# Kernel tuning notes

Measured on AMD Instinct MI355X. Metric: run time of the kernel, lower is better.

## Reference

```python
import math
import jax, jax.numpy as jnp
import numpy as np

L, H, K, NH, V, DFF = 6, 512, 512, 8, 64, 1024
B, T, S = 8, 512, 512
PAD = 0


def _ln(x, g, b, eps=1e-5):
    m = jnp.mean(x, -1, keepdims=True)
    v = jnp.mean((x - m) ** 2, -1, keepdims=True)
    return (x - m) * jax.lax.rsqrt(v + eps) * g + b


def _mha(Q, Kin, Vin, mask, wq, bq, wk, bk, wv, bv, wo, bo, g, b):
    # weights stored [in, out]
    B_, Tq, Hd = Q.shape
    dk = wq.shape[1] // NH
    dv = wv.shape[1] // NH
    q = (Q @ wq + bq).reshape(B_, Tq, NH, dk).transpose(0, 2, 1, 3)
    k = (Kin @ wk + bk).reshape(B_, -1, NH, dk).transpose(0, 2, 1, 3)
    v = (Vin @ wv + bv).reshape(B_, -1, NH, dv).transpose(0, 2, 1, 3)
    scores = jnp.einsum('bhqd,bhkd->bhqk', q, k) / jnp.sqrt(jnp.float32(dk))
    scores = jnp.where(mask[:, None, :, :], jnp.float32(-1e9), scores)
    attn = jax.nn.softmax(scores, axis=-1)
    ctx = jnp.einsum('bhqk,bhkd->bhqd', attn, v).transpose(0, 2, 1, 3).reshape(B_, Tq, Hd)
    return _ln(ctx @ wo + bo + Q, g, b)


def _pe(t, d):
    pos = jnp.arange(t, dtype=jnp.float32)[:, None]
    div = jnp.exp(jnp.arange(0, d, 2, dtype=jnp.float32) * (-math.log(10000.0) / d))
    pe = jnp.zeros((t, d), jnp.float32)
    pe = pe.at[:, 0::2].set(jnp.sin(pos * div)).at[:, 1::2].set(jnp.cos(pos * div))
    return pe


def setup_inputs() -> dict:
    key = jax.random.key(0)
    ks = iter(jax.random.split(key, 40))
    nrm = lambda shape, s=0.02: jax.random.normal(next(ks), shape, jnp.float32) * s
    inp = {
        'smiles_index': jax.random.randint(next(ks), (B, T), 0, V, dtype=jnp.int32),
        'enc_outputs': jax.random.normal(next(ks), (B, S, H), jnp.float32),
        'enc_pad_mask': jnp.zeros((B, 1, S), bool),
        'tgt_len': T,
        'mol_emb': nrm((V, H), 1.0).at[PAD].set(0.0),  # padding_idx=0 row zeroed
        # self-attn stacks [L, ...]
        'sa_wq': nrm((L, H, K)), 'sa_bq': jnp.zeros((L, K)),
        'sa_wk': nrm((L, H, K)), 'sa_bk': jnp.zeros((L, K)),
        'sa_wv': nrm((L, H, H)), 'sa_bv': jnp.zeros((L, H)),
        'sa_wo': nrm((L, H, H)), 'sa_bo': jnp.zeros((L, H)),
        'ln1_g': jnp.ones((L, H)), 'ln1_b': jnp.zeros((L, H)),
        # cross-attn stacks
        'ea_wq': nrm((L, H, K)), 'ea_bq': jnp.zeros((L, K)),
        'ea_wk': nrm((L, H, K)), 'ea_bk': jnp.zeros((L, K)),
        'ea_wv': nrm((L, H, H)), 'ea_bv': jnp.zeros((L, H)),
        'ea_wo': nrm((L, H, H)), 'ea_bo': jnp.zeros((L, H)),
        'ln2_g': jnp.ones((L, H)), 'ln2_b': jnp.zeros((L, H)),
        # conv1x1 FFN == per-position linear
        'c1_w': nrm((L, H, DFF)), 'c1_b': jnp.zeros((L, DFF)),
        'c2_w': nrm((L, DFF, H)), 'c2_b': jnp.zeros((L, H)),
        'ln3_g': jnp.ones((L, H)), 'ln3_b': jnp.zeros((L, H)),
    }
    return inp


def reference(smiles_index, enc_outputs, enc_pad_mask, tgt_len, mol_emb,
              sa_wq, sa_bq, sa_wk, sa_bk, sa_wv, sa_bv, sa_wo, sa_bo, ln1_g, ln1_b,
              ea_wq, ea_bq, ea_wk, ea_bk, ea_wv, ea_bv, ea_wo, ea_bo, ln2_g, ln2_b,
              c1_w, c1_b, c2_w, c2_b, ln3_g, ln3_b):
    b, t = smiles_index.shape
    s = enc_outputs.shape[1]
    # embeddings + sinusoidal positional encoding (dropout is identity in eval)
    x = mol_emb[smiles_index] + _pe(t, mol_emb.shape[1])[None]
    # masks: pad (key == pad_id) OR causal upper-triangular
    pad = (smiles_index == PAD)[:, None, :]                 # [B,1,T] -> broadcast over queries
    causal = jnp.triu(jnp.ones((t, t), bool), 1)[None]      # [1,T,T]
    self_mask = pad | causal                                # [B,T,T]
    enc_mask = jnp.broadcast_to(enc_pad_mask, (b, t, s))    # [B,T,S]
    for l in range(L):
        x = _mha(x, x, x, self_mask,
                 sa_wq[l], sa_bq[l], sa_wk[l], sa_bk[l], sa_wv[l], sa_bv[l],
                 sa_wo[l], sa_bo[l], ln1_g[l], ln1_b[l])
        x = _mha(x, enc_outputs, enc_outputs, enc_mask,
                 ea_wq[l], ea_bq[l], ea_wk[l], ea_bk[l], ea_wv[l], ea_bv[l],
                 ea_wo[l], ea_bo[l], ln2_g[l], ln2_b[l])
        h = jax.nn.relu(x @ c1_w[l] + c1_b[l])
        y = h @ c2_w[l] + c2_b[l]
        x = _ln(y + x, ln3_g[l], ln3_b[l])
    return x
```

## Files before the change

### kernel.cpp

```cpp
#include <hip/hip_runtime.h>
#include <hip/hip_bf16.h>
#include <math.h>

#define NL   6
#define HD   512
#define NHD  8
#define DK   64
#define DFFN 1024
#define NB   8
#define TT   512
#define MROWS (NB*TT)

typedef __hip_bfloat16 bf16;
typedef __attribute__((ext_vector_type(8))) short short8v;
typedef __attribute__((ext_vector_type(4))) float f32x4;

__device__ __forceinline__ float wave_sum(float v) {
#pragma unroll
  for (int off = 32; off; off >>= 1) v += __shfl_xor(v, off);
  return v;
}
__device__ __forceinline__ unsigned short f2bf(float x) {
  __hip_bfloat16 h = __float2bfloat16(x);
  return *reinterpret_cast<unsigned short*>(&h);
}

__global__ __launch_bounds__(256)
void wprep_kernel(const float* __restrict__ W, bf16* __restrict__ Wt, int Kd, int Nd) {
  __shared__ float t[32][33];
  const size_t mo = (size_t)blockIdx.z * Kd * Nd;
  const int n0 = blockIdx.x * 32, k0 = blockIdx.y * 32;
  const int tx = threadIdx.x & 31, ty = threadIdx.x >> 5;
#pragma unroll
  for (int j = 0; j < 4; ++j)
    t[ty + j * 8][tx] = W[mo + (size_t)(k0 + ty + j * 8) * Nd + n0 + tx];
  __syncthreads();
#pragma unroll
  for (int j = 0; j < 4; ++j)
    Wt[mo + (size_t)(n0 + ty + j * 8) * Kd + k0 + tx] = __float2bfloat16(t[tx][ty + j * 8]);
}

__global__ __launch_bounds__(256)
void cvtbf16_kernel(const float* __restrict__ in, unsigned short* __restrict__ out) {
  const int i = (blockIdx.x * 256 + threadIdx.x) * 4;
  float4 v = *(const float4*)(in + i);
  out[i + 0] = f2bf(v.x); out[i + 1] = f2bf(v.y);
  out[i + 2] = f2bf(v.z); out[i + 3] = f2bf(v.w);
}

__global__ __launch_bounds__(256)
void embed_pe_kernel(const int* __restrict__ idx, const float* __restrict__ emb,
                     float* __restrict__ x, unsigned short* __restrict__ xb) {
  const int row = blockIdx.x;
  const int t = row & (TT - 1);
  const int tok = idx[row];
  const float cdiv = -0.017988946009466842f;
#pragma unroll
  for (int e0 = 0; e0 < 2; ++e0) {
    const int e = threadIdx.x + e0 * 256;
    const float div = __expf((float)(e & ~1) * cdiv);
    const float ang = (float)t * div;
    const float pe = (e & 1) ? cosf(ang) : sinf(ang);
    const float v = emb[(size_t)tok * HD + e] + pe;
    x[(size_t)row * HD + e] = v;
    xb[(size_t)row * HD + e] = f2bf(v);
  }
}

__device__ __forceinline__ void gemm_compute(const char* As, const char* Bs,
                                             int wm, int wn, int lane,
                                             f32x4 (&acc)[2][2]) {
  const int rsw = (lane & 7) << 4;
  const int csel = (lane >> 4) * 16;
  short8v af[2][2], bfr[2][2];
#pragma unroll
  for (int m = 0; m < 2; ++m)
#pragma unroll
    for (int kk = 0; kk < 2; ++kk) {
      const int row = wm * 32 + m * 16 + (lane & 15);
      af[m][kk] = *(const short8v*)(As + row * 128 + ((kk * 64 + csel) ^ rsw));
    }
#pragma unroll
  for (int n = 0; n < 2; ++n)
#pragma unroll
    for (int kk = 0; kk < 2; ++kk) {
      const int row = wn * 32 + n * 16 + (lane & 15);
      bfr[n][kk] = *(const short8v*)(Bs + row * 128 + ((kk * 64 + csel) ^ rsw));
    }
#pragma unroll
  for (int m = 0; m < 2; ++m)
#pragma unroll
    for (int n = 0; n < 2; ++n) {
      acc[m][n] = __builtin_amdgcn_mfma_f32_16x16x32_bf16(af[m][0], bfr[n][0], acc[m][n], 0, 0, 0);
      acc[m][n] = __builtin_amdgcn_mfma_f32_16x16x32_bf16(af[m][1], bfr[n][1], acc[m][n], 0, 0, 0);
    }
}

template<int OUT_BF16, int RELU>
__global__ __launch_bounds__(256)
void mgemm_kernel(const bf16* __restrict__ A, const bf16* __restrict__ Bt,
                  const float* __restrict__ bias, float* __restrict__ Cf,
                  unsigned short* __restrict__ Cb, int M, int N, int K) {
  __shared__ __attribute__((aligned(16))) char As[64 * 128];
  __shared__ __attribute__((aligned(16))) char Bs[64 * 128];

  const int tid = threadIdx.x;
  const int w = tid >> 6, lane = tid & 63;
  const int wm = w >> 1, wn = w & 1;
  const int m0 = blockIdx.x * 64, n0 = blockIdx.y * 64;

  const int sr = w * 16 + (lane >> 3);
  const int scol = (lane & 7) * 16;
  const int swc = scol ^ ((sr & 7) << 4);
  const bf16* ga0 = A + (size_t)(m0 + sr) * K + (scol >> 1);
  const bf16* ga1 = A + (size_t)(m0 + sr + 8) * K + (scol >> 1);
  const bf16* gb0 = Bt + (size_t)(n0 + sr) * K + (scol >> 1);
  const bf16* gb1 = Bt + (size_t)(n0 + sr + 8) * K + (scol >> 1);
  char* la0 = As + sr * 128 + swc;
  char* la1 = As + (sr + 8) * 128 + swc;
  char* lb0 = Bs + sr * 128 + swc;
  char* lb1 = Bs + (sr + 8) * 128 + swc;

  f32x4 acc[2][2] = {};

  short8v ra0 = *(const short8v*)ga0, ra1 = *(const short8v*)ga1;
  short8v rb0 = *(const short8v*)gb0, rb1 = *(const short8v*)gb1;
  short8v sa0, sa1, sb0, sb1;

  for (int k0 = 0; k0 < K; k0 += 128) {
    __syncthreads();
    *(short8v*)la0 = ra0; *(short8v*)la1 = ra1;
    *(short8v*)lb0 = rb0; *(short8v*)lb1 = rb1;
    __syncthreads();
    sa0 = *(const short8v*)(ga0 + k0 + 64); sa1 = *(const short8v*)(ga1 + k0 + 64);
    sb0 = *(const short8v*)(gb0 + k0 + 64); sb1 = *(const short8v*)(gb1 + k0 + 64);
    gemm_compute(As, Bs, wm, wn, lane, acc);
    __syncthreads();
    *(short8v*)la0 = sa0; *(short8v*)la1 = sa1;
    *(short8v*)lb0 = sb0; *(short8v*)lb1 = sb1;
    __syncthreads();
    if (k0 + 128 < K) {
      ra0 = *(const short8v*)(ga0 + k0 + 128); ra1 = *(const short8v*)(ga1 + k0 + 128);
      rb0 = *(const short8v*)(gb0 + k0 + 128); rb1 = *(const short8v*)(gb1 + k0 + 128);
    }
    gemm_compute(As, Bs, wm, wn, lane, acc);
  }

  const int crow = (lane >> 4) * 4;
  const int ccol = lane & 15;
#pragma unroll
  for (int m = 0; m < 2; ++m)
#pragma unroll
    for (int n = 0; n < 2; ++n) {
      const int gr = m0 + wm * 32 + m * 16 + crow;
      const int gc = n0 + wn * 32 + n * 16 + ccol;
      const float bs = bias[gc];
#pragma unroll
      for (int r = 0; r < 4; ++r) {
        float v = acc[m][n][r] + bs;
        if (RELU) v = fmaxf(v, 0.f);
        if (OUT_BF16) Cb[(size_t)(gr + r) * N + gc] = f2bf(v);
        else          Cf[(size_t)(gr + r) * N + gc] = v;
      }
    }
}

template<int CAUSAL>
__global__ __launch_bounds__(256)
void mattn_kernel(const unsigned short* __restrict__ q, const unsigned short* __restrict__ kgl,
                  const unsigned short* __restrict__ vgl, unsigned short* __restrict__ ctx,
                  const int* __restrict__ idx, const unsigned char* __restrict__ emask) {
  __shared__ __attribute__((aligned(16))) unsigned short kt[64 * 64];
  __shared__ __attribute__((aligned(16))) unsigned short vt[64 * 64];
  __shared__ __attribute__((aligned(16))) unsigned short pl[4][16 * 64];
  __shared__ float km[64];

  const int bh = blockIdx.x;
  const int b = bh >> 3, h = bh & 7;
  const int qbase = blockIdx.y * 64;
  const int tid = threadIdx.x, w = tid >> 6, lane = tid & 63;
  const int l4 = lane & 15, g = lane >> 4;

  const unsigned short* qp = q + (size_t)(b * TT + qbase + w * 16 + l4) * HD + h * DK + g * 8;
  short8v aq0 = *(const short8v*)qp;
  short8v aq1 = *(const short8v*)(qp + 32);

  float m_r[4], l_r[4];
  f32x4 acc_o[4];
#pragma unroll
  for (int r = 0; r < 4; ++r) { m_r[r] = -1e30f; l_r[r] = 0.f; }
#pragma unroll
  for (int f = 0; f < 4; ++f) acc_o[f] = (f32x4){0.f, 0.f, 0.f, 0.f};

  const int kvEnd = CAUSAL ? (qbase + 64) : TT;
  for (int kt0 = 0; kt0 < kvEnd; kt0 += 64) {
    __syncthreads();
    if (tid < 64) {
      const int kp = b * TT + kt0 + tid;
      const bool mk = CAUSAL ? (idx[kp] == 0) : (emask[kp] != 0);
      km[tid] = mk ? 1.f : 0.f;
    }
    {
      const int r = tid >> 2;
      const int bc = (tid & 3) * 32;
      const unsigned short* kp = kgl + (size_t)(b * TT + kt0 + r) * HD + h * DK + (bc >> 1);
      short8v ka = *(const short8v*)kp;
      short8v kb2 = *(const short8v*)(kp + 8);
      const int sw = (r & 7) << 4;
      *(short8v*)((char*)kt + r * 128 + (bc ^ sw)) = ka;
      *(short8v*)((char*)kt + r * 128 + ((bc + 16) ^ sw)) = kb2;
    }
    {
      const int k2 = (tid & 31) * 2;
      const int d0 = (tid >> 5) * 8;
      const unsigned short* vp0 = vgl + (size_t)(b * TT + kt0 + k2) * HD + h * DK + d0;
      const unsigned short* vp1 = vp0 + HD;
      short8v v0 = *(const short8v*)vp0;
      short8v v1 = *(const short8v*)vp1;
#pragma unroll
      for (int j = 0; j < 8; ++j) {
        const int d = d0 + j;
        const unsigned pk = ((unsigned)(unsigned short)v0[j]) | (((unsigned)(unsigned short)v1[j]) << 16);
        *(unsigned*)((char*)vt + d * 128 + ((k2 * 2) ^ ((d & 7) << 4))) = pk;
      }
    }
    __syncthreads();

    f32x4 s4[4];
#pragma unroll
    for (int f = 0; f < 4; ++f) {
      const int krow = f * 16 + l4;
      const int sw = (krow & 7) << 4;
      short8v bk0 = *(const short8v*)((const char*)kt + krow * 128 + ((g * 16) ^ sw));
      short8v bk1 = *(const short8v*)((const char*)kt + krow * 128 + ((64 + g * 16) ^ sw));
      f32x4 a = {};
      a = __builtin_amdgcn_mfma_f32_16x16x32_bf16(aq0, bk0, a, 0, 0, 0);
      a = __builtin_amdgcn_mfma_f32_16x16x32_bf16(aq1, bk1, a, 0, 0, 0);
      s4[f] = a;
    }

    float sc_r[4];
#pragma unroll
    for (int r = 0; r < 4; ++r) {
      const int qpos = qbase + w * 16 + g * 4 + r;
      float sf[4];
#pragma unroll
      for (int f = 0; f < 4; ++f) {
        const int kpos = kt0 + f * 16 + l4;
        float s = s4[f][r] * 0.125f;
        const bool msk = (km[f * 16 + l4] != 0.f) || (CAUSAL && kpos > qpos);
        sf[f] = msk ? -1e9f : s;
      }
      float mx = fmaxf(fmaxf(sf[0], sf[1]), fmaxf(sf[2], sf[3]));
#pragma unroll
      for (int off = 8; off; off >>= 1) mx = fmaxf(mx, __shfl_xor(mx, off));
      const float mn = fmaxf(m_r[r], mx);
      const float sc = __expf(m_r[r] - mn);
      m_r[r] = mn;
      sc_r[r] = sc;
      float ps = 0.f;
      const int prow = g * 4 + r;
      const int psw = (prow & 7) << 4;
#pragma unroll
      for (int f = 0; f < 4; ++f) {
        const float p = __expf(sf[f] - mn);
        ps += p;
        *(unsigned short*)((char*)pl[w] + prow * 128 + ((f * 32 + l4 * 2) ^ psw)) = f2bf(p);
      }
#pragma unroll
      for (int off = 8; off; off >>= 1) ps += __shfl_xor(ps, off);
      l_r[r] = l_r[r] * sc + ps;
    }

#pragma unroll
    for (int f = 0; f < 4; ++f)
#pragma unroll
      for (int r = 0; r < 4; ++r) acc_o[f][r] *= sc_r[r];

    const int asw = (l4 & 7) << 4;
    short8v pa0 = *(const short8v*)((const char*)pl[w] + l4 * 128 + ((g * 16) ^ asw));
    short8v pa1 = *(const short8v*)((const char*)pl[w] + l4 * 128 + ((g * 16 + 64) ^ asw));
#pragma unroll
    for (int f = 0; f < 4; ++f) {
      const int drow = f * 16 + l4;
      const int sw = (drow & 7) << 4;
      short8v vb0 = *(const short8v*)((const char*)vt + drow * 128 + ((g * 16) ^ sw));
      short8v vb1 = *(const short8v*)((const char*)vt + drow * 128 + ((g * 16 + 64) ^ sw));
      acc_o[f] = __builtin_amdgcn_mfma_f32_16x16x32_bf16(pa0, vb0, acc_o[f], 0, 0, 0);
      acc_o[f] = __builtin_amdgcn_mfma_f32_16x16x32_bf16(pa1, vb1, acc_o[f], 0, 0, 0);
    }
  }

  float rl[4];
#pragma unroll
  for (int r = 0; r < 4; ++r) rl[r] = 1.f / l_r[r];
#pragma unroll
  for (int f = 0; f < 4; ++f)
#pragma unroll
    for (int r = 0; r < 4; ++r) {
      const int row = qbase + w * 16 + g * 4 + r;
      const int col = h * DK + f * 16 + l4;
      ctx[(size_t)(b * TT + row) * HD + col] = f2bf(acc_o[f][r] * rl[r]);
    }
}

__global__ __launch_bounds__(256)
void ln_kernel(const float* __restrict__ y, const float* __restrict__ res,
               float* __restrict__ out, unsigned short* __restrict__ outb,
               const float* __restrict__ g, const float* __restrict__ bta) {
  const int row = blockIdx.x;
  const int tid = threadIdx.x;
  const int w = tid >> 6, lane = tid & 63;
  const float* yr = y + (size_t)row * HD;
  const float* rr = res + (size_t)row * HD;

  float v0 = yr[tid] + rr[tid];
  float v1 = yr[tid + 256] + rr[tid + 256];

  __shared__ float red[4];
  float s = wave_sum(v0 + v1);
  if (lane == 0) red[w] = s;
  __syncthreads();
  const float mean = (red[0] + red[1] + red[2] + red[3]) * (1.f / HD);
  __syncthreads();

  const float d0 = v0 - mean, d1 = v1 - mean;
  float qv = wave_sum(d0 * d0 + d1 * d1);
  if (lane == 0) red[w] = qv;
  __syncthreads();
  const float var = (red[0] + red[1] + red[2] + red[3]) * (1.f / HD);
  const float rstd = rsqrtf(var + 1e-5f);

  const float o0 = d0 * rstd * g[tid] + bta[tid];
  const float o1 = d1 * rstd * g[tid + 256] + bta[tid + 256];
  out[(size_t)row * HD + tid] = o0;
  out[(size_t)row * HD + tid + 256] = o1;
  outb[(size_t)row * HD + tid] = f2bf(o0);
  outb[(size_t)row * HD + tid + 256] = f2bf(o1);
}

extern "C" void kernel_launch(void* const* d_in, const int* in_sizes, int n_in,
                              void* d_out, int out_size, void* d_ws, size_t ws_size,
                              hipStream_t stream) {
  const int* idx = (const int*)d_in[0];
  const float* enc = (const float*)d_in[1];
  const unsigned char* emask = (const unsigned char*)d_in[2];
  const float* emb = (const float*)d_in[4];
  const float* sa_wq = (const float*)d_in[5];
  const float* sa_bq = (const float*)d_in[6];
  const float* sa_wk = (const float*)d_in[7];
  const float* sa_bk = (const float*)d_in[8];
  const float* sa_wv = (const float*)d_in[9];
  const float* sa_bv = (const float*)d_in[10];
  const float* sa_wo = (const float*)d_in[11];
  const float* sa_bo = (const float*)d_in[12];
  const float* ln1g = (const float*)d_in[13];
  const float* ln1b = (const float*)d_in[14];
  const float* ea_wq = (const float*)d_in[15];
  const float* ea_bq = (const float*)d_in[16];
  const float* ea_wk = (const float*)d_in[17];
  const float* ea_bk = (const float*)d_in[18];
  const float* ea_wv = (const float*)d_in[19];
  const float* ea_bv = (const float*)d_in[20];
  const float* ea_wo = (const float*)d_in[21];
  const float* ea_bo = (const float*)d_in[22];
  const float* ln2g = (const float*)d_in[23];
  const float* ln2b = (const float*)d_in[24];
  const float* c1w = (const float*)d_in[25];
  const float* c1b = (const float*)d_in[26];
  const float* c2w = (const float*)d_in[27];
  const float* c2b = (const float*)d_in[28];
  const float* ln3g = (const float*)d_in[29];
  const float* ln3b = (const float*)d_in[30];

  const size_t MH = (size_t)MROWS * HD;
  const size_t SQ = (size_t)HD * HD;
  char* ws = (char*)d_ws;
  float*          x    = (float*)(ws + 0);
  unsigned short* xb   = (unsigned short*)(ws + (8u << 20));
  unsigned short* qb   = (unsigned short*)(ws + (12u << 20));
  unsigned short* kb   = (unsigned short*)(ws + (16u << 20));
  unsigned short* vb   = (unsigned short*)(ws + (20u << 20));
  float*          yb   = (float*)(ws + (24u << 20));
  unsigned short* cxb  = (unsigned short*)(ws + (32u << 20));
  unsigned short* encb = (unsigned short*)(ws + (36u << 20));
  bf16*           wt   = (bf16*)(ws + (40u << 20));
  unsigned short* hb   = qb;

  bf16* t_sa_q = wt;
  bf16* t_sa_k = wt + 6 * SQ;
  bf16* t_sa_v = wt + 12 * SQ;
  bf16* t_sa_o = wt + 18 * SQ;
  bf16* t_ea_q = wt + 24 * SQ;
  bf16* t_ea_k = wt + 30 * SQ;
  bf16* t_ea_v = wt + 36 * SQ;
  bf16* t_ea_o = wt + 42 * SQ;
  bf16* t_c1   = wt + 48 * SQ;
  bf16* t_c2   = wt + 48 * SQ + 12 * SQ;

  const dim3 blk(256);
  const dim3 g512(MROWS / 64, HD / 64);
  const dim3 gFF(MROWS / 64, DFFN / 64);
  const dim3 attng(NB * NHD, TT / 64);

  wprep_kernel<<<dim3(16, 16, NL), blk, 0, stream>>>(sa_wq, t_sa_q, HD, HD);
  wprep_kernel<<<dim3(16, 16, NL), blk, 0, stream>>>(sa_wk, t_sa_k, HD, HD);
  wprep_kernel<<<dim3(16, 16, NL), blk, 0, stream>>>(sa_wv, t_sa_v, HD, HD);
  wprep_kernel<<<dim3(16, 16, NL), blk, 0, stream>>>(sa_wo, t_sa_o, HD, HD);
  wprep_kernel<<<dim3(16, 16, NL), blk, 0, stream>>>(ea_wq, t_ea_q, HD, HD);
  wprep_kernel<<<dim3(16, 16, NL), blk, 0, stream>>>(ea_wk, t_ea_k, HD, HD);
  wprep_kernel<<<dim3(16, 16, NL), blk, 0, stream>>>(ea_wv, t_ea_v, HD, HD);
  wprep_kernel<<<dim3(16, 16, NL), blk, 0, stream>>>(ea_wo, t_ea_o, HD, HD);
  wprep_kernel<<<dim3(32, 16, NL), blk, 0, stream>>>(c1w, t_c1, HD, DFFN);
  wprep_kernel<<<dim3(16, 32, NL), blk, 0, stream>>>(c2w, t_c2, DFFN, HD);
  cvtbf16_kernel<<<MH / 1024, blk, 0, stream>>>(enc, encb);

  embed_pe_kernel<<<MROWS, blk, 0, stream>>>(idx, emb, x, xb);

  for (int l = 0; l < NL; ++l) {
    const size_t wo = (size_t)l * SQ;
    const size_t b512 = (size_t)l * HD;
    const size_t w1 = (size_t)l * HD * DFFN;
    const size_t bFF = (size_t)l * DFFN;

    mgemm_kernel<1, 0><<<g512, blk, 0, stream>>>((const bf16*)xb, t_sa_q + wo, sa_bq + b512, nullptr, qb, MROWS, HD, HD);
    mgemm_kernel<1, 0><<<g512, blk, 0, stream>>>((const bf16*)xb, t_sa_k + wo, sa_bk + b512, nullptr, kb, MROWS, HD, HD);
    mgemm_kernel<1, 0><<<g512, blk, 0, stream>>>((const bf16*)xb, t_sa_v + wo, sa_bv + b512, nullptr, vb, MROWS, HD, HD);
    mattn_kernel<1><<<attng, blk, 0, stream>>>(qb, kb, vb, cxb, idx, emask);
    mgemm_kernel<0, 0><<<g512, blk, 0, stream>>>((const bf16*)cxb, t_sa_o + wo, sa_bo + b512, yb, nullptr, MROWS, HD, HD);
    ln_kernel<<<MROWS, blk, 0, stream>>>(yb, x, x, xb, ln1g + b512, ln1b + b512);

    mgemm_kernel<1, 0><<<g512, blk, 0, stream>>>((const bf16*)xb, t_ea_q + wo, ea_bq + b512, nullptr, qb, MROWS, HD, HD);
    mgemm_kernel<1, 0><<<g512, blk, 0, stream>>>((const bf16*)encb, t_ea_k + wo, ea_bk + b512, nullptr, kb, MROWS, HD, HD);
    mgemm_kernel<1, 0><<<g512, blk, 0, stream>>>((const bf16*)encb, t_ea_v + wo, ea_bv + b512, nullptr, vb, MROWS, HD, HD);
    mattn_kernel<0><<<attng, blk, 0, stream>>>(qb, kb, vb, cxb, idx, emask);
    mgemm_kernel<0, 0><<<g512, blk, 0, stream>>>((const bf16*)cxb, t_ea_o + wo, ea_bo + b512, yb, nullptr, MROWS, HD, HD);
    ln_kernel<<<MROWS, blk, 0, stream>>>(yb, x, x, xb, ln2g + b512, ln2b + b512);

    mgemm_kernel<1, 1><<<gFF, blk, 0, stream>>>((const bf16*)xb, t_c1 + w1, c1b + bFF, nullptr, hb, MROWS, DFFN, HD);
    mgemm_kernel<0, 0><<<g512, blk, 0, stream>>>((const bf16*)hb, t_c2 + w1, c2b + b512, yb, nullptr, MROWS, HD, DFFN);
    ln_kernel<<<MROWS, blk, 0, stream>>>(yb, x, x, xb, ln3g + b512, ln3b + b512);
  }

  hipMemcpyAsync(d_out, x, MH * sizeof(float), hipMemcpyDeviceToDevice, stream);
}
```

Measured before the change: 926.8 us.

## Fuse QKV and cross-attn KV projections and use larger async-LDS GEMM tiles

```diff
diff --git a/kernel.cpp b/kernel.cpp
--- a/kernel.cpp
+++ b/kernel.cpp
@@ -25,19 +25,40 @@
   return *reinterpret_cast<unsigned short*>(&h);
 }
 
-__global__ __launch_bounds__(256)
-void wprep_kernel(const float* __restrict__ W, bf16* __restrict__ Wt, int Kd, int Nd) {
+__device__ __forceinline__ void gload16(const void* g, void* l) {
+  __builtin_amdgcn_global_load_lds(
+      (const __attribute__((address_space(1))) unsigned int*)g,
+      (__attribute__((address_space(3))) unsigned int*)l, 16, 0, 0);
+}
+
+__global__ __launch_bounds__(256)
+void wprep_kernel(const float* __restrict__ W, bf16* __restrict__ Wt, int Kd, int Nd,
+                  int dstRowOff, int dstSlabRows) {
   __shared__ float t[32][33];
-  const size_t mo = (size_t)blockIdx.z * Kd * Nd;
+  const size_t src = (size_t)blockIdx.z * Kd * Nd;
+  const size_t dst = (size_t)blockIdx.z * dstSlabRows * Kd;
   const int n0 = blockIdx.x * 32, k0 = blockIdx.y * 32;
   const int tx = threadIdx.x & 31, ty = threadIdx.x >> 5;
 #pragma unroll
   for (int j = 0; j < 4; ++j)
-    t[ty + j * 8][tx] = W[mo + (size_t)(k0 + ty + j * 8) * Nd + n0 + tx];
+    t[ty + j * 8][tx] = W[src + (size_t)(k0 + ty + j * 8) * Nd + n0 + tx];
   __syncthreads();
 #pragma unroll
   for (int j = 0; j < 4; ++j)
-    Wt[mo + (size_t)(n0 + ty + j * 8) * Kd + k0 + tx] = __float2bfloat16(t[tx][ty + j * 8]);
+    Wt[dst + (size_t)(dstRowOff + n0 + ty + j * 8) * Kd + k0 + tx] =
+        __float2bfloat16(t[tx][ty + j * 8]);
+}
+
+__global__ __launch_bounds__(256)
+void bcat_kernel(const float* __restrict__ b0, const float* __restrict__ b1,
+                 const float* __restrict__ b2, float* __restrict__ out, int nseg) {
+  const int l = blockIdx.x;
+  const int stride = 512 * nseg;
+  for (int i = threadIdx.x; i < stride; i += 256) {
+    const int seg = i >> 9, off = i & 511;
+    const float* src = seg == 0 ? b0 : (seg == 1 ? b1 : b2);
+    out[(size_t)l * stride + i] = src[(size_t)l * 512 + off];
+  }
 }
 
 __global__ __launch_bounds__(256)
@@ -67,100 +88,92 @@
   }
 }
 
-__device__ __forceinline__ void gemm_compute(const char* As, const char* Bs,
-                                             int wm, int wn, int lane,
-                                             f32x4 (&acc)[2][2]) {
-  const int rsw = (lane & 7) << 4;
-  const int csel = (lane >> 4) * 16;
-  short8v af[2][2], bfr[2][2];
-#pragma unroll
-  for (int m = 0; m < 2; ++m)
+template<int TN, int OUT_BF16, int RELU>
+__global__ __launch_bounds__(256)
+void mgemm2_kernel(const bf16* __restrict__ A, const bf16* __restrict__ Bt,
+                   const float* __restrict__ bias, float* __restrict__ Cf,
+                   unsigned short* __restrict__ Cb, int M, int N, int K) {
+  constexpr int NR = TN / 32;
+  constexpr int BJ = TN / 32;
+  __shared__ __attribute__((aligned(16))) char As[2][128 * 128];
+  __shared__ __attribute__((aligned(16))) char Bs[2][TN * 128];
+
+  const int tid = threadIdx.x, w = tid >> 6, lane = tid & 63;
+  const int wm = w >> 1, wn = w & 1;
+  const int m0 = blockIdx.x * 128, n0 = blockIdx.y * TN;
+  const int lrow = lane >> 3;
+  const int lchk = (lane & 7) ^ lrow;
+
+  const bf16* ga[4];
+#pragma unroll
+  for (int j = 0; j < 4; ++j)
+    ga[j] = A + (size_t)(m0 + w * 32 + j * 8 + lrow) * K + lchk * 8;
+  const bf16* gb[BJ];
+#pragma unroll
+  for (int j = 0; j < BJ; ++j)
+    gb[j] = Bt + (size_t)(n0 + w * (8 * BJ) + j * 8 + lrow) * K + lchk * 8;
+
+  f32x4 acc[4][NR];
+#pragma unroll
+  for (int fm = 0; fm < 4; ++fm)
+#pragma unroll
+    for (int fn = 0; fn < NR; ++fn) acc[fm][fn] = (f32x4){0.f, 0.f, 0.f, 0.f};
+
+  const int l4 = lane & 15;
+  const int khb = (lane >> 4) * 16;
+
+  auto issue = [&](int t, int buf) {
+#pragma unroll
+    for (int j = 0; j < 4; ++j)
+      gload16(ga[j] + t * 64, &As[buf][(w * 32 + j * 8) * 128]);
+#pragma unroll
+    for (int j = 0; j < BJ; ++j)
+      gload16(gb[j] + t * 64, &Bs[buf][(w * (8 * BJ) + j * 8) * 128]);
+  };
+  auto compute = [&](int buf) {
 #pragma unroll
     for (int kk = 0; kk < 2; ++kk) {
-      const int row = wm * 32 + m * 16 + (lane & 15);
-      af[m][kk] = *(const short8v*)(As + row * 128 + ((kk * 64 + csel) ^ rsw));
-    }
-#pragma unroll
-  for (int n = 0; n < 2; ++n)
-#pragma unroll
-    for (int kk = 0; kk < 2; ++kk) {
-      const int row = wn * 32 + n * 16 + (lane & 15);
-      bfr[n][kk] = *(const short8v*)(Bs + row * 128 + ((kk * 64 + csel) ^ rsw));
-    }
-#pragma unroll
-  for (int m = 0; m < 2; ++m)
-#pragma unroll
-    for (int n = 0; n < 2; ++n) {
-      acc[m][n] = __builtin_amdgcn_mfma_f32_16x16x32_bf16(af[m][0], bfr[n][0], acc[m][n], 0, 0, 0);
-      acc[m][n] = __builtin_amdgcn_mfma_f32_16x16x32_bf16(af[m][1], bfr[n][1], acc[m][n], 0, 0, 0);
-    }
-}
-
-template<int OUT_BF16, int RELU>
-__global__ __launch_bounds__(256)
-void mgemm_kernel(const bf16* __restrict__ A, const bf16* __restrict__ Bt,
-                  const float* __restrict__ bias, float* __restrict__ Cf,
-                  unsigned short* __restrict__ Cb, int M, int N, int K) {
-  __shared__ __attribute__((aligned(16))) char As[64 * 128];
-  __shared__ __attribute__((aligned(16))) char Bs[64 * 128];
-
-  const int tid = threadIdx.x;
-  const int w = tid >> 6, lane = tid & 63;
-  const int wm = w >> 1, wn = w & 1;
-  const int m0 = blockIdx.x * 64, n0 = blockIdx.y * 64;
-
-  const int sr = w * 16 + (lane >> 3);
-  const int scol = (lane & 7) * 16;
-  const int swc = scol ^ ((sr & 7) << 4);
-  const bf16* ga0 = A + (size_t)(m0 + sr) * K + (scol >> 1);
-  const bf16* ga1 = A + (size_t)(m0 + sr + 8) * K + (scol >> 1);
-  const bf16* gb0 = Bt + (size_t)(n0 + sr) * K + (scol >> 1);
-  const bf16* gb1 = Bt + (size_t)(n0 + sr + 8) * K + (scol >> 1);
-  char* la0 = As + sr * 128 + swc;
-  char* la1 = As + (sr + 8) * 128 + swc;
-  char* lb0 = Bs + sr * 128 + swc;
-  char* lb1 = Bs + (sr + 8) * 128 + swc;
-
-  f32x4 acc[2][2] = {};
-
-  short8v ra0 = *(const short8v*)ga0, ra1 = *(const short8v*)ga1;
-  short8v rb0 = *(const short8v*)gb0, rb1 = *(const short8v*)gb1;
-  short8v sa0, sa1, sb0, sb1;
-
-  for (int k0 = 0; k0 < K; k0 += 128) {
+      short8v af[4], bfv[NR];
+#pragma unroll
+      for (int fm = 0; fm < 4; ++fm) {
+        const int r = wm * 64 + fm * 16 + l4;
+        af[fm] = *(const short8v*)(&As[buf][r * 128 + ((kk * 64 + khb) ^ ((r & 7) << 4))]);
+      }
+#pragma unroll
+      for (int fn = 0; fn < NR; ++fn) {
+        const int r = wn * (TN / 2) + fn * 16 + l4;
+        bfv[fn] = *(const short8v*)(&Bs[buf][r * 128 + ((kk * 64 + khb) ^ ((r & 7) << 4))]);
+      }
+#pragma unroll
+      for (int fm = 0; fm < 4; ++fm)
+#pragma unroll
+        for (int fn = 0; fn < NR; ++fn)
+          acc[fm][fn] = __builtin_amdgcn_mfma_f32_16x16x32_bf16(af[fm], bfv[fn], acc[fm][fn], 0, 0, 0);
+    }
+  };
+
+  const int NT = K >> 6;
+  issue(0, 0);
+  for (int t = 0; t < NT; ++t) {
     __syncthreads();
-    *(short8v*)la0 = ra0; *(short8v*)la1 = ra1;
-    *(short8v*)lb0 = rb0; *(short8v*)lb1 = rb1;
-    __syncthreads();
-    sa0 = *(const short8v*)(ga0 + k0 + 64); sa1 = *(const short8v*)(ga1 + k0 + 64);
-    sb0 = *(const short8v*)(gb0 + k0 + 64); sb1 = *(const short8v*)(gb1 + k0 + 64);
-    gemm_compute(As, Bs, wm, wn, lane, acc);
-    __syncthreads();
-    *(short8v*)la0 = sa0; *(short8v*)la1 = sa1;
-    *(short8v*)lb0 = sb0; *(short8v*)lb1 = sb1;
-    __syncthreads();
-    if (k0 + 128 < K) {
-      ra0 = *(const short8v*)(ga0 + k0 + 128); ra1 = *(const short8v*)(ga1 + k0 + 128);
-      rb0 = *(const short8v*)(gb0 + k0 + 128); rb1 = *(const short8v*)(gb1 + k0 + 128);
-    }
-    gemm_compute(As, Bs, wm, wn, lane, acc);
+    if (t + 1 < NT) issue(t + 1, (t + 1) & 1);
+    compute(t & 1);
   }
 
-  const int crow = (lane >> 4) * 4;
-  const int ccol = lane & 15;
-#pragma unroll
-  for (int m = 0; m < 2; ++m)
-#pragma unroll
-    for (int n = 0; n < 2; ++n) {
-      const int gr = m0 + wm * 32 + m * 16 + crow;
-      const int gc = n0 + wn * 32 + n * 16 + ccol;
+  const int crow = (lane >> 4) * 4, ccol = l4;
+#pragma unroll
+  for (int fm = 0; fm < 4; ++fm)
+#pragma unroll
+    for (int fn = 0; fn < NR; ++fn) {
+      const int gr = m0 + wm * 64 + fm * 16 + crow;
+      const int gc = n0 + wn * (TN / 2) + fn * 16 + ccol;
       const float bs = bias[gc];
 #pragma unroll
       for (int r = 0; r < 4; ++r) {
-        float v = acc[m][n][r] + bs;
-        if (RELU) v = fmaxf(v, 0.f);
-        if (OUT_BF16) Cb[(size_t)(gr + r) * N + gc] = f2bf(v);
-        else          Cf[(size_t)(gr + r) * N + gc] = v;
+        float vv = acc[fm][fn][r] + bs;
+        if (RELU) vv = fmaxf(vv, 0.f);
+        if (OUT_BF16) Cb[(size_t)(gr + r) * N + gc] = f2bf(vv);
+        else          Cf[(size_t)(gr + r) * N + gc] = vv;
       }
     }
 }
@@ -169,7 +182,8 @@
 __global__ __launch_bounds__(256)
 void mattn_kernel(const unsigned short* __restrict__ q, const unsigned short* __restrict__ kgl,
                   const unsigned short* __restrict__ vgl, unsigned short* __restrict__ ctx,
-                  const int* __restrict__ idx, const unsigned char* __restrict__ emask) {
+                  const int* __restrict__ idx, const unsigned char* __restrict__ emask,
+                  int qstride, int kvstride) {
   __shared__ __attribute__((aligned(16))) unsigned short kt[64 * 64];
   __shared__ __attribute__((aligned(16))) unsigned short vt[64 * 64];
   __shared__ __attribute__((aligned(16))) unsigned short pl[4][16 * 64];
@@ -181,7 +195,7 @@
   const int tid = threadIdx.x, w = tid >> 6, lane = tid & 63;
   const int l4 = lane & 15, g = lane >> 4;
 
-  const unsigned short* qp = q + (size_t)(b * TT + qbase + w * 16 + l4) * HD + h * DK + g * 8;
+  const unsigned short* qp = q + (size_t)(b * TT + qbase + w * 16 + l4) * qstride + h * DK + g * 8;
   short8v aq0 = *(const short8v*)qp;
   short8v aq1 = *(const short8v*)(qp + 32);
 
@@ -203,7 +217,7 @@
     {
       const int r = tid >> 2;
       const int bc = (tid & 3) * 32;
-      const unsigned short* kp = kgl + (size_t)(b * TT + kt0 + r) * HD + h * DK + (bc >> 1);
+      const unsigned short* kp = kgl + (size_t)(b * TT + kt0 + r) * kvstride + h * DK + (bc >> 1);
       short8v ka = *(const short8v*)kp;
       short8v kb2 = *(const short8v*)(kp + 8);
       const int sw = (r & 7) << 4;
@@ -213,8 +227,8 @@
     {
       const int k2 = (tid & 31) * 2;
       const int d0 = (tid >> 5) * 8;
-      const unsigned short* vp0 = vgl + (size_t)(b * TT + kt0 + k2) * HD + h * DK + d0;
-      const unsigned short* vp1 = vp0 + HD;
+      const unsigned short* vp0 = vgl + (size_t)(b * TT + kt0 + k2) * kvstride + h * DK + d0;
+      const unsigned short* vp1 = vp0 + kvstride;
       short8v v0 = *(const short8v*)vp0;
       short8v v1 = *(const short8v*)vp1;
 #pragma unroll
@@ -378,67 +392,75 @@
   char* ws = (char*)d_ws;
   float*          x    = (float*)(ws + 0);
   unsigned short* xb   = (unsigned short*)(ws + (8u << 20));
-  unsigned short* qb   = (unsigned short*)(ws + (12u << 20));
-  unsigned short* kb   = (unsigned short*)(ws + (16u << 20));
-  unsigned short* vb   = (unsigned short*)(ws + (20u << 20));
-  float*          yb   = (float*)(ws + (24u << 20));
-  unsigned short* cxb  = (unsigned short*)(ws + (32u << 20));
-  unsigned short* encb = (unsigned short*)(ws + (36u << 20));
-  bf16*           wt   = (bf16*)(ws + (40u << 20));
-  unsigned short* hb   = qb;
-
-  bf16* t_sa_q = wt;
-  bf16* t_sa_k = wt + 6 * SQ;
-  bf16* t_sa_v = wt + 12 * SQ;
-  bf16* t_sa_o = wt + 18 * SQ;
-  bf16* t_ea_q = wt + 24 * SQ;
-  bf16* t_ea_k = wt + 30 * SQ;
-  bf16* t_ea_v = wt + 36 * SQ;
-  bf16* t_ea_o = wt + 42 * SQ;
-  bf16* t_c1   = wt + 48 * SQ;
-  bf16* t_c2   = wt + 48 * SQ + 12 * SQ;
+  unsigned short* qkvb = (unsigned short*)(ws + (12u << 20));
+  unsigned short* qcb  = (unsigned short*)(ws + (24u << 20));
+  unsigned short* kvb  = (unsigned short*)(ws + (28u << 20));
+  unsigned short* cxb  = (unsigned short*)(ws + (36u << 20));
+  float*          yb   = (float*)(ws + (40u << 20));
+  unsigned short* encb = (unsigned short*)(ws + (48u << 20));
+  bf16*           wt   = (bf16*)(ws + (52u << 20));
+  float*          bcS  = (float*)(ws + (92u << 20));
+  float*          bcKV = (float*)(ws + (93u << 20));
+  unsigned short* hb   = qkvb;
+
+  bf16* t_saqkv = wt;
+  bf16* t_sao   = wt + 18 * SQ;
+  bf16* t_eaq   = wt + 24 * SQ;
+  bf16* t_eakv  = wt + 30 * SQ;
+  bf16* t_eao   = wt + 42 * SQ;
+  bf16* t_c1    = wt + 48 * SQ;
+  bf16* t_c2    = wt + 60 * SQ;
 
   const dim3 blk(256);
-  const dim3 g512(MROWS / 64, HD / 64);
-  const dim3 gFF(MROWS / 64, DFFN / 64);
+  const dim3 gQKV(MROWS / 128, 1536 / 128);
+  const dim3 g1024(MROWS / 128, 1024 / 128);
+  const dim3 g512n(MROWS / 128, 512 / 64);
   const dim3 attng(NB * NHD, TT / 64);
 
-  wprep_kernel<<<dim3(16, 16, NL), blk, 0, stream>>>(sa_wq, t_sa_q, HD, HD);
-  wprep_kernel<<<dim3(16, 16, NL), blk, 0, stream>>>(sa_wk, t_sa_k, HD, HD);
-  wprep_kernel<<<dim3(16, 16, NL), blk, 0, stream>>>(sa_wv, t_sa_v, HD, HD);
-  wprep_kernel<<<dim3(16, 16, NL), blk, 0, stream>>>(sa_wo, t_sa_o, HD, HD);
-  wprep_kernel<<<dim3(16, 16, NL), blk, 0, stream>>>(ea_wq, t_ea_q, HD, HD);
-  wprep_kernel<<<dim3(16, 16, NL), blk, 0, stream>>>(ea_wk, t_ea_k, HD, HD);
-  wprep_kernel<<<dim3(16, 16, NL), blk, 0, stream>>>(ea_wv, t_ea_v, HD, HD);
-  wprep_kernel<<<dim3(16, 16, NL), blk, 0, stream>>>(ea_wo, t_ea_o, HD, HD);
-  wprep_kernel<<<dim3(32, 16, NL), blk, 0, stream>>>(c1w, t_c1, HD, DFFN);
-  wprep_kernel<<<dim3(16, 32, NL), blk, 0, stream>>>(c2w, t_c2, DFFN, HD);
+  wprep_kernel<<<dim3(16, 16, NL), blk, 0, stream>>>(sa_wq, t_saqkv, HD, HD, 0, 1536);
+  wprep_kernel<<<dim3(16, 16, NL), blk, 0, stream>>>(sa_wk, t_saqkv, HD, HD, 512, 1536);
+  wprep_kernel<<<dim3(16, 16, NL), blk, 0, stream>>>(sa_wv, t_saqkv, HD, HD, 1024, 1536);
+  wprep_kernel<<<dim3(16, 16, NL), blk, 0, stream>>>(sa_wo, t_sao, HD, HD, 0, 512);
+  wprep_kernel<<<dim3(16, 16, NL), blk, 0, stream>>>(ea_wq, t_eaq, HD, HD, 0, 512);
+  wprep_kernel<<<dim3(16, 16, NL), blk, 0, stream>>>(ea_wk, t_eakv, HD, HD, 0, 1024);
+  wprep_kernel<<<dim3(16, 16, NL), blk, 0, stream>>>(ea_wv, t_eakv, HD, HD, 512, 1024);
+  wprep_kernel<<<dim3(16, 16, NL), blk, 0, stream>>>(ea_wo, t_eao, HD, HD, 0, 512);
+  wprep_kernel<<<dim3(32, 16, NL), blk, 0, stream>>>(c1w, t_c1, HD, DFFN, 0, 1024);
+  wprep_kernel<<<dim3(16, 32, NL), blk, 0, stream>>>(c2w, t_c2, DFFN, HD, 0, 512);
+  bcat_kernel<<<NL, blk, 0, stream>>>(sa_bq, sa_bk, sa_bv, bcS, 3);
+  bcat_kernel<<<NL, blk, 0, stream>>>(ea_bk, ea_bv, nullptr, bcKV, 2);
   cvtbf16_kernel<<<MH / 1024, blk, 0, stream>>>(enc, encb);
 
   embed_pe_kernel<<<MROWS, blk, 0, stream>>>(idx, emb, x, xb);
 
   for (int l = 0; l < NL; ++l) {
-    const size_t wo = (size_t)l * SQ;
     const size_t b512 = (size_t)l * HD;
-    const size_t w1 = (size_t)l * HD * DFFN;
     const size_t bFF = (size_t)l * DFFN;
 
-    mgemm_kernel<1, 0><<<g512, blk, 0, stream>>>((const bf16*)xb, t_sa_q + wo, sa_bq + b512, nullptr, qb, MROWS, HD, HD);
-    mgemm_kernel<1, 0><<<g512, blk, 0, stream>>>((const bf16*)xb, t_sa_k + wo, sa_bk + b512, nullptr, kb, MROWS, HD, HD);
-    mgemm_kernel<1, 0><<<g512, blk, 0, stream>>>((const bf16*)xb, t_sa_v + wo, sa_bv + b512, nullptr, vb, MROWS, HD, HD);
-    mattn_kernel<1><<<attng, blk, 0, stream>>>(qb, kb, vb, cxb, idx, emask);
-    mgemm_kernel<0, 0><<<g512, blk, 0, stream>>>((const bf16*)cxb, t_sa_o + wo, sa_bo + b512, yb, nullptr, MROWS, HD, HD);
+    mgemm2_kernel<128, 1, 0><<<gQKV, blk, 0, stream>>>(
+        (const bf16*)xb, t_saqkv + (size_t)l * 3 * SQ, bcS + (size_t)l * 1536,
+        nullptr, qkvb, MROWS, 1536, HD);
+    mattn_kernel<1><<<attng, blk, 0, stream>>>(qkvb, qkvb + 512, qkvb + 1024, cxb,
+                                               idx, emask, 1536, 1536);
+    mgemm2_kernel<64, 0, 0><<<g512n, blk, 0, stream>>>(
+        (const bf16*)cxb, t_sao + (size_t)l * SQ, sa_bo + b512, yb, nullptr, MROWS, HD, HD);
     ln_kernel<<<MROWS, blk, 0, stream>>>(yb, x, x, xb, ln1g + b512, ln1b + b512);
 
-    mgemm_kernel<1, 0><<<g512, blk, 0, stream>>>((const bf16*)xb, t_ea_q + wo, ea_bq + b512, nullptr, qb, MROWS, HD, HD);
-    mgemm_kernel<1, 0><<<g512, blk, 0, stream>>>((const bf16*)encb, t_ea_k + wo, ea_bk + b512, nullptr, kb, MROWS, HD, HD);
-    mgemm_kernel<1, 0><<<g512, blk, 0, stream>>>((const bf16*)encb, t_ea_v + wo, ea_bv + b512, nullptr, vb, MROWS, HD, HD);
-    mattn_kernel<0><<<attng, blk, 0, stream>>>(qb, kb, vb, cxb, idx, emask);
-    mgemm_kernel<0, 0><<<g512, blk, 0, stream>>>((const bf16*)cxb, t_ea_o + wo, ea_bo + b512, yb, nullptr, MROWS, HD, HD);
+    mgemm2_kernel<64, 1, 0><<<g512n, blk, 0, stream>>>(
+        (const bf16*)xb, t_eaq + (size_t)l * SQ, ea_bq + b512, nullptr, qcb, MROWS, HD, HD);
+    mgemm2_kernel<128, 1, 0><<<g1024, blk, 0, stream>>>(
+        (const bf16*)encb, t_eakv + (size_t)l * 2 * SQ, bcKV + (size_t)l * 1024,
+        nullptr, kvb, MROWS, 1024, HD);
+    mattn_kernel<0><<<attng, blk, 0, stream>>>(qcb, kvb, kvb + 512, cxb,
+                                               idx, emask, 512, 1024);
+    mgemm2_kernel<64, 0, 0><<<g512n, blk, 0, stream>>>(
+        (const bf16*)cxb, t_eao + (size_t)l * SQ, ea_bo + b512, yb, nullptr, MROWS, HD, HD);
     ln_kernel<<<MROWS, blk, 0, stream>>>(yb, x, x, xb, ln2g + b512, ln2b + b512);
 
-    mgemm_kernel<1, 1><<<gFF, blk, 0, stream>>>((const bf16*)xb, t_c1 + w1, c1b + bFF, nullptr, hb, MROWS, DFFN, HD);
-    mgemm_kernel<0, 0><<<g512, blk, 0, stream>>>((const bf16*)hb, t_c2 + w1, c2b + b512, yb, nullptr, MROWS, HD, DFFN);
+    mgemm2_kernel<128, 1, 1><<<g1024, blk, 0, stream>>>(
+        (const bf16*)xb, t_c1 + (size_t)l * 2 * SQ, c1b + bFF, nullptr, hb, MROWS, DFFN, HD);
+    mgemm2_kernel<64, 0, 0><<<g512n, blk, 0, stream>>>(
+        (const bf16*)hb, t_c2 + (size_t)l * 2 * SQ, c2b + b512, yb, nullptr, MROWS, HD, DFFN);
     ln_kernel<<<MROWS, blk, 0, stream>>>(yb, x, x, xb, ln3g + b512, ln3b + b512);
   }
 
```

Result: no change. 941.8 us (+1.6%).
